# Optimization experiments

Measured on AMD Instinct MI355X. Metric: run time of the kernel, lower is better.

Reference implementation:

```python
import jax, jax.numpy as jnp
import numpy as np

N_NODES = 100000
N_EDGES = 1600000
NODE_DIM = 16
EDGE_DIM = 16
OUT_DIM = 16
H = 64  # edge/node/global hidden size
N_GRAPHS = 1


def _glorot(key, shape):
    fan_in, fan_out = shape[0], shape[1]
    lim = np.sqrt(6.0 / (fan_in + fan_out))
    return jax.random.uniform(key, shape, jnp.float32, -lim, lim)


def setup_inputs() -> dict:
    key = jax.random.key(0)
    ks = jax.random.split(key, 16)
    x = jax.random.normal(ks[0], (N_NODES, NODE_DIM), jnp.float32)
    edge_attr = jax.random.normal(ks[1], (N_EDGES, EDGE_DIM), jnp.float32)
    u = jax.random.normal(ks[2], (N_GRAPHS, H), jnp.float32)
    senders = jax.random.randint(ks[3], (N_EDGES,), 0, N_NODES, jnp.int32)
    receivers = jax.random.randint(ks[4], (N_EDGES,), 0, N_NODES, jnp.int32)
    node_gidx = jnp.zeros((N_NODES,), jnp.int32)
    edge_gidx = jnp.zeros((N_EDGES,), jnp.int32)
    # EdgeBlock MLP: in = edge + 2*node + global_h
    W_eb = _glorot(ks[5], (EDGE_DIM + 2 * NODE_DIM + H, H)); b_eb = jnp.zeros((H,), jnp.float32)
    # NodeBlock MLP: in = node + edge_h + global_h
    W_nb = _glorot(ks[6], (NODE_DIM + H + H, H)); b_nb = jnp.zeros((H,), jnp.float32)
    # GlobalBlock MLP: in = node_h + edge_h + global_h
    W_gb = _glorot(ks[7], (H + H + H, H)); b_gb = jnp.zeros((H,), jnp.float32)
    # node decoder: in = 2*edge_h + node_h + global_h -> H -> out
    W_d1 = _glorot(ks[8], (2 * H + H + H, H)); b_d1 = jnp.zeros((H,), jnp.float32)
    W_d2 = _glorot(ks[9], (H, OUT_DIM)); b_d2 = jnp.zeros((OUT_DIM,), jnp.float32)
    return dict(x=x, edge_attr=edge_attr, u=u, senders=senders, receivers=receivers,
                node_gidx=node_gidx, edge_gidx=edge_gidx,
                W_eb=W_eb, b_eb=b_eb, W_nb=W_nb, b_nb=b_nb, W_gb=W_gb, b_gb=b_gb,
                W_d1=W_d1, b_d1=b_d1, W_d2=W_d2, b_d2=b_d2)


def _segment_mean(data, ids, num_segments):
    s = jax.ops.segment_sum(data, ids, num_segments=num_segments)
    cnt = jax.ops.segment_sum(jnp.ones((data.shape[0], 1), data.dtype), ids, num_segments=num_segments)
    return s / jnp.maximum(cnt, 1.0)


def reference(x, edge_attr, u, senders, receivers, node_gidx, edge_gidx,
              W_eb, b_eb, W_nb, b_nb, W_gb, b_gb, W_d1, b_d1, W_d2, b_d2):
    # ---- GN1: EdgeBlock (gather -> concat -> linear+relu) ----
    e_in = jnp.concatenate([edge_attr, x[receivers], x[senders], u[edge_gidx]], axis=-1)  # [E, 112]
    e_h = jax.nn.relu(e_in @ W_eb + b_eb)  # [E, H]
    # ---- GN1: NodeBlock (scatter_add of received edges) ----
    agg_recv = jax.ops.segment_sum(e_h, receivers, num_segments=x.shape[0])  # [N, H]
    n_in = jnp.concatenate([agg_recv, x, u[node_gidx]], axis=-1)
    n_h = jax.nn.relu(n_in @ W_nb + b_nb)  # [N, H]
    # ---- GN1: GlobalBlock (scatter_mean reductions) ----
    e_mean = _segment_mean(e_h, edge_gidx, u.shape[0])  # [B, H]
    n_mean = _segment_mean(n_h, node_gidx, u.shape[0])  # [B, H]
    g_in = jnp.concatenate([e_mean, n_mean, u], axis=-1)
    u2 = jax.nn.relu(g_in @ W_gb + b_gb)  # [B, H]
    # ---- GN2: node decoder block (scatter_mean sent + received edges) ----
    agg_recv2 = _segment_mean(e_h, receivers, x.shape[0])
    agg_sent2 = _segment_mean(e_h, senders, x.shape[0])
    d_in = jnp.concatenate([agg_recv2, agg_sent2, n_h, u2[node_gidx]], axis=-1)  # [N, 256]
    out = jax.nn.relu(d_in @ W_d1 + b_d1) @ W_d2 + b_d2  # [N, out_dim]
    return out
```

## Files before the change

kernel.cpp:

```cpp
#include <hip/hip_runtime.h>


typedef unsigned int uint;
typedef unsigned short ushort;
typedef __attribute__((ext_vector_type(8))) short bf16x8;
typedef __attribute__((ext_vector_type(4))) float f32x4;

#define BW 128
#define BSHIFT 7
#define NBMAX 784
#define DC 8192
#define EMASK 0x1FFFFFu

#define LDF4(p) (*reinterpret_cast<const float4*>(p))

__device__ __forceinline__ ushort f2bf(float f) {
  uint u = __float_as_uint(f);
  u += 0x7FFFu + ((u >> 16) & 1u);
  return (ushort)(u >> 16);
}

__device__ __forceinline__ int aswz(int row, int kb) {
  return row * 64 + ((kb ^ (row & 7)) << 3);
}
__device__ __forceinline__ int nswz(int row, int kb) {
  return row * 128 + (((kb & 8) | ((kb ^ row) & 7)) << 3);
}
__device__ __forceinline__ int aswz192(int row, int kb) {
  return row * 192 + (((kb & 24) | ((kb ^ row) & 7)) << 3);
}

__global__ __launch_bounds__(256) void init_kernel(
    const float* __restrict__ x, ushort* __restrict__ xb, int n16,
    const float* __restrict__ u, const float* __restrict__ W_eb,
    const float* __restrict__ b_eb, const float* __restrict__ W_nb,
    const float* __restrict__ b_nb, const float* __restrict__ W_d1,
    const float* __restrict__ W_d2, float* __restrict__ eb_init,
    float* __restrict__ nb_init, ushort* __restrict__ wt_lin,
    ushort* __restrict__ wnb_img, ushort* __restrict__ wtd1_img,
    ushort* __restrict__ w2_img) {
  if (blockIdx.x == 0) {
    int j = threadIdx.x;
    if (j >= 64) return;
    float ae = b_eb[j], an = b_nb[j];
    for (int k = 0; k < 64; ++k) {
      float uk = u[k];
      ae = fmaf(uk, W_eb[(48 + k) * 64 + j], ae);
      an = fmaf(uk, W_nb[(80 + k) * 64 + j], an);
    }
    eb_init[j] = ae;
    nb_init[j] = an;
    for (int k = 0; k < 64; ++k)
      wt_lin[j * 64 + k] = (k < 48) ? f2bf(W_eb[k * 64 + j]) : (ushort)0;
    for (int k = 0; k < 128; ++k) {
      ushort v = (k < 80) ? f2bf(W_nb[k * 64 + j]) : (ushort)0;
      wnb_img[nswz(j, k >> 3) + (k & 7)] = v;
    }
    for (int k = 0; k < 192; ++k)
      wtd1_img[aswz192(j, k >> 3) + (k & 7)] = f2bf(W_d1[k * 64 + j]);
    if (j < 16)
      for (int k = 0; k < 64; ++k)
        w2_img[aswz(j, k >> 3) + (k & 7)] = f2bf(W_d2[k * 16 + j]);
    return;
  }
  int i = (blockIdx.x - 1) * 256 + threadIdx.x;
  if (i * 4 >= n16) return;
  float4 a = LDF4(x + i * 4);
  ushort4 o = {f2bf(a.x), f2bf(a.y), f2bf(a.z), f2bf(a.w)};
  *reinterpret_cast<ushort4*>(xb + i * 4) = o;
}

__global__ __launch_bounds__(256) void bcount_kernel(
    const int* __restrict__ receivers, const int* __restrict__ senders,
    uint* __restrict__ bcnt_r, uint* __restrict__ bcnt_s, int E, int NB) {
  __shared__ uint hr[NBMAX], hs[NBMAX];
  int t = threadIdx.x;
  for (int i = t; i < NB; i += 256) { hr[i] = 0; hs[i] = 0; }
  __syncthreads();
  int stride = gridDim.x * 256;
  for (int e = blockIdx.x * 256 + t; e < E; e += stride) {
    atomicAdd(&hr[receivers[e] >> BSHIFT], 1u);
    atomicAdd(&hs[senders[e] >> BSHIFT], 1u);
  }
  __syncthreads();
  for (int i = t; i < NB; i += 256) {
    if (hr[i]) atomicAdd(&bcnt_r[i], hr[i]);
    if (hs[i]) atomicAdd(&bcnt_s[i], hs[i]);
  }
}

__global__ __launch_bounds__(256) void bscan_kernel(
    const uint* __restrict__ bcnt_r, const uint* __restrict__ bcnt_s,
    uint* __restrict__ start_r, uint* __restrict__ start_s,
    uint* __restrict__ cur_r, uint* __restrict__ cur_s, int E, int NB) {
  __shared__ uint ts[256];
  int t = threadIdx.x;
  #pragma unroll
  for (int pass = 0; pass < 2; ++pass) {
    const uint* cnt = pass ? bcnt_s : bcnt_r;
    uint* start = pass ? start_s : start_r;
    uint* cur = pass ? cur_s : cur_r;
    uint loc[4]; uint tsum = 0;
    #pragma unroll
    for (int q = 0; q < 4; ++q) {
      int i = t * 4 + q;
      loc[q] = (i < NB) ? cnt[i] : 0;
      tsum += loc[q];
    }
    ts[t] = tsum;
    __syncthreads();
    for (int off = 1; off < 256; off <<= 1) {
      uint a = (t >= off) ? ts[t - off] : 0;
      __syncthreads();
      ts[t] += a;
      __syncthreads();
    }
    uint run = ts[t] - tsum;
    #pragma unroll
    for (int q = 0; q < 4; ++q) {
      int i = t * 4 + q;
      if (i < NB) { start[i] = run; cur[i] = run; run += loc[q]; }
    }
    if (t == 0) start[NB] = (uint)E;
    __syncthreads();
  }
}

__global__ __launch_bounds__(256) void distribute_kernel(
    const int* __restrict__ receivers, const int* __restrict__ senders,
    uint* __restrict__ gcur_r, uint* __restrict__ gcur_s,
    uint* __restrict__ tmp_r, uint* __restrict__ tmp_s, int E, int NB) {
  __shared__ uint hist[NBMAX], lstart[NBMAX], cur[NBMAX], gbase[NBMAX];
  __shared__ uint ids[DC];
  __shared__ ushort idsB[DC];
  __shared__ uint ts[256];
  int dir = blockIdx.x & 1;
  const int* key = dir ? senders : receivers;
  uint* g_cursor = dir ? gcur_s : gcur_r;
  uint* tmp = dir ? tmp_s : tmp_r;
  int t = threadIdx.x;
  int base = (blockIdx.x >> 1) * DC;
  int cact = min(DC, E - base);
  for (int i = t; i < NB; i += 256) hist[i] = 0;
  __syncthreads();
  for (int k = 0; k < DC / 256; ++k) {
    int j = k * 256 + t;
    if (j < cact) atomicAdd(&hist[key[base + j] >> BSHIFT], 1u);
  }
  __syncthreads();
  {
    uint loc[4]; uint tsum = 0;
    #pragma unroll
    for (int q = 0; q < 4; ++q) {
      int i = t * 4 + q;
      loc[q] = (i < NB) ? hist[i] : 0;
      tsum += loc[q];
    }
    ts[t] = tsum;
    __syncthreads();
    for (int off = 1; off < 256; off <<= 1) {
      uint a = (t >= off) ? ts[t - off] : 0;
      __syncthreads();
      ts[t] += a;
      __syncthreads();
    }
    uint run = ts[t] - tsum;
    #pragma unroll
    for (int q = 0; q < 4; ++q) {
      int i = t * 4 + q;
      if (i < NB) { lstart[i] = run; cur[i] = run; run += loc[q]; }
    }
  }
  __syncthreads();
  for (int i = t; i < NB; i += 256)
    if (hist[i]) gbase[i] = atomicAdd(&g_cursor[i], hist[i]);
  for (int k = 0; k < DC / 256; ++k) {
    int j = k * 256 + t;
    if (j < cact) {
      int e = base + j;
      int kk = key[e];
      uint b = (uint)(kk >> BSHIFT);
      uint slot = atomicAdd(&cur[b], 1u);
      ids[slot] = ((uint)(kk & (BW - 1)) << 21) | (uint)e;
      idsB[slot] = (ushort)b;
    }
  }
  __syncthreads();
  for (int j = t; j < cact; j += 256) {
    uint b2 = idsB[j];
    tmp[gbase[b2] + ((uint)j - lstart[b2])] = ids[j];
  }
}

__global__ __launch_bounds__(256) void bucketsort_kernel(
    const uint* __restrict__ tmp_r, const uint* __restrict__ tmp_s,
    const uint* __restrict__ start_r, const uint* __restrict__ start_s,
    uint* __restrict__ eidx_r, uint* __restrict__ eidx_s,
    uint* __restrict__ cnt_r, uint* __restrict__ cnt_s, int N) {
  __shared__ uint hist[BW], pfx[BW], cur[BW];
  int d = blockIdx.x & 1;
  int b = blockIdx.x >> 1;
  const uint* tmp = d ? tmp_s : tmp_r;
  const uint* start = d ? start_s : start_r;
  uint* eidx = d ? eidx_s : eidx_r;
  uint* cnt = d ? cnt_s : cnt_r;
  int t = threadIdx.x;
  if (t < BW) hist[t] = 0;
  __syncthreads();
  int beg = (int)start[b], end = (int)start[b + 1];
  for (int i = beg + t; i < end; i += 256) atomicAdd(&hist[tmp[i] >> 21], 1u);
  __syncthreads();
  if (t < BW) pfx[t] = hist[t];
  __syncthreads();
  for (int off = 1; off < BW; off <<= 1) {
    uint a = 0;
    if (t < BW && t >= off) a = pfx[t - off];
    __syncthreads();
    if (t < BW) pfx[t] += a;
    __syncthreads();
  }
  if (t < BW) cur[t] = pfx[t] - hist[t];
  __syncthreads();
  for (int i = beg + t; i < end; i += 256) {
    uint v = tmp[i];
    uint nl = v >> 21;
    uint p = atomicAdd(&cur[nl], 1u);
    eidx[beg + p] = v & EMASK;
  }
  int nbase = b * BW;
  if (t < BW && nbase + t < N) cnt[nbase + t] = hist[t];
}

__global__ __launch_bounds__(256, 4) void escatter_kernel(
    const float* __restrict__ edge_attr, const ushort* __restrict__ xb,
    const int* __restrict__ senders, const int* __restrict__ receivers,
    const uint* __restrict__ eidx_r, const uint* __restrict__ eidx_s,
    const ushort* __restrict__ wt_lin, const float* __restrict__ eb_init,
    float* __restrict__ sum_recv, float* __restrict__ sum_sent, int E,
    int ntiles) {
  __shared__ float Clds[4][16 * 72];
  __shared__ int nodeW[4][16];
  int t = threadIdx.x;
  int wid = t >> 6, l = t & 63;
  int lrow = l & 15, lk = l >> 4;
  bf16x8 b0[4], b1[4];
  float ebi[4];
  #pragma unroll
  for (int nt = 0; nt < 4; ++nt) {
    const ushort* wr = wt_lin + (nt * 16 + lrow) * 64;
    b0[nt] = *reinterpret_cast<const bf16x8*>(wr + lk * 8);
    b1[nt] = *reinterpret_cast<const bf16x8*>(wr + 32 + lk * 8);
    ebi[nt] = eb_init[nt * 16 + lrow];
  }
  const bf16x8 zero8 = {0, 0, 0, 0, 0, 0, 0, 0};
  int dir = blockIdx.x & 1;
  const uint* eidx = dir ? eidx_s : eidx_r;
  float* sum = dir ? sum_sent : sum_recv;
  int gw = (blockIdx.x >> 1) * 4 + wid;
  int nw = (gridDim.x >> 1) * 4;
  for (int tile = gw; tile < ntiles; tile += nw) {
    int m = tile * 16 + lrow;
    int mc = min(m, E - 1);
    int e = (int)eidx[mc];
    int r = receivers[e];
    int s = senders[e];
    if (lk == 0) nodeW[wid][lrow] = dir ? s : r;
    bf16x8 a0, a1;
    if (lk < 2) {
      const float* ap = edge_attr + (size_t)e * 16 + lk * 8;
      float4 f0 = LDF4(ap), f1 = LDF4(ap + 4);
      union { ushort h[8]; bf16x8 v; } pk;
      pk.h[0] = f2bf(f0.x); pk.h[1] = f2bf(f0.y);
      pk.h[2] = f2bf(f0.z); pk.h[3] = f2bf(f0.w);
      pk.h[4] = f2bf(f1.x); pk.h[5] = f2bf(f1.y);
      pk.h[6] = f2bf(f1.z); pk.h[7] = f2bf(f1.w);
      a0 = pk.v;
      a1 = *reinterpret_cast<const bf16x8*>(xb + (size_t)s * 16 + lk * 8);
    } else {
      a0 = *reinterpret_cast<const bf16x8*>(xb + (size_t)r * 16 +
                                            (lk - 2) * 8);
      a1 = zero8;
    }
    f32x4 acc[4];
    #pragma unroll
    for (int nt = 0; nt < 4; ++nt) {
      acc[nt] = f32x4{ebi[nt], ebi[nt], ebi[nt], ebi[nt]};
      acc[nt] =
          __builtin_amdgcn_mfma_f32_16x16x32_bf16(a0, b0[nt], acc[nt], 0, 0, 0);
      acc[nt] =
          __builtin_amdgcn_mfma_f32_16x16x32_bf16(a1, b1[nt], acc[nt], 0, 0, 0);
    }
    int m0 = (l >> 4) * 4;
    #pragma unroll
    for (int nt = 0; nt < 4; ++nt) {
      #pragma unroll
      for (int reg = 0; reg < 4; ++reg) {
        Clds[wid][(m0 + reg) * 72 + nt * 16 + lrow] =
            fmaxf(acc[nt][reg], 0.f);
      }
    }
    int vc = min(16, E - tile * 16);
    float accum = 0.f;
    int prev = nodeW[wid][0];
    for (int mm = 0; mm < vc; ++mm) {
      int nd = nodeW[wid][mm];
      float v = Clds[wid][mm * 72 + l];
      if (nd != prev) {
        atomicAdd(&sum[(size_t)prev * 64 + l], accum);
        accum = 0.f;
        prev = nd;
      }
      accum += v;
    }
    atomicAdd(&sum[(size_t)prev * 64 + l], accum);
  }
}

__global__ __launch_bounds__(256, 2) void node_mfma_kernel(
    const float* __restrict__ sum_recv, const ushort* __restrict__ xb,
    const ushort* __restrict__ wnb_img, const float* __restrict__ nb_init,
    ushort* __restrict__ n_h, int N) {
  __shared__ ushort Alds[64 * 128];
  __shared__ ushort Wlds[64 * 128];
  __shared__ ushort Clds[4][16 * 72];
  int t = threadIdx.x;
  int base = blockIdx.x * 64;
  {
    const uint4* src = reinterpret_cast<const uint4*>(wnb_img);
    uint4* dst = reinterpret_cast<uint4*>(Wlds);
    #pragma unroll
    for (int i = 0; i < 4; ++i) dst[t + 256 * i] = src[t + 256 * i];
  }
  {
    int m = t >> 2, part = t & 3;
    int n = base + m;
    bool val = n < N;
    if (part < 2) {
      #pragma unroll
      for (int q = 0; q < 4; ++q) {
        int c = part * 4 + q;
        union { ushort h[8]; uint4 qq; } pk;
        if (val) {
          const float* src = sum_recv + (size_t)n * 64 + c * 8;
          float4 f0 = LDF4(src), f1 = LDF4(src + 4);
          pk.h[0] = f2bf(f0.x); pk.h[1] = f2bf(f0.y);
          pk.h[2] = f2bf(f0.z); pk.h[3] = f2bf(f0.w);
          pk.h[4] = f2bf(f1.x); pk.h[5] = f2bf(f1.y);
          pk.h[6] = f2bf(f1.z); pk.h[7] = f2bf(f1.w);
        } else {
          pk.qq = uint4{0, 0, 0, 0};
        }
        *reinterpret_cast<uint4*>(&Alds[nswz(m, c)]) = pk.qq;
      }
    } else if (part == 2) {
      uint4 w0 = {0, 0, 0, 0}, w1 = {0, 0, 0, 0};
      if (val) {
        const uint4* xp = reinterpret_cast<const uint4*>(xb + (size_t)n * 16);
        w0 = xp[0]; w1 = xp[1];
      }
      *reinterpret_cast<uint4*>(&Alds[nswz(m, 8)]) = w0;
      *reinterpret_cast<uint4*>(&Alds[nswz(m, 9)]) = w1;
      *reinterpret_cast<uint4*>(&Alds[nswz(m, 10)]) = uint4{0, 0, 0, 0};
      *reinterpret_cast<uint4*>(&Alds[nswz(m, 11)]) = uint4{0, 0, 0, 0};
    } else {
      #pragma unroll
      for (int q = 0; q < 4; ++q)
        *reinterpret_cast<uint4*>(&Alds[nswz(m, 12 + q)]) = uint4{0, 0, 0, 0};
    }
  }
  __syncthreads();
  int wid = t >> 6, l = t & 63;
  int lrow = l & 15, lk = l >> 4;
  int arow = wid * 16 + lrow;
  bf16x8 afr[4];
  #pragma unroll
  for (int g = 0; g < 4; ++g)
    afr[g] = *reinterpret_cast<const bf16x8*>(&Alds[nswz(arow, g * 4 + lk)]);
  f32x4 acc[4];
  #pragma unroll
  for (int nt = 0; nt < 4; ++nt) {
    float nbi = nb_init[nt * 16 + lrow];
    acc[nt] = f32x4{nbi, nbi, nbi, nbi};
    #pragma unroll
    for (int g = 0; g < 4; ++g) {
      bf16x8 b = *reinterpret_cast<const bf16x8*>(
          &Wlds[nswz(nt * 16 + lrow, g * 4 + lk)]);
      acc[nt] =
          __builtin_amdgcn_mfma_f32_16x16x32_bf16(afr[g], b, acc[nt], 0, 0, 0);
    }
  }
  int m0 = (l >> 4) * 4;
  #pragma unroll
  for (int nt = 0; nt < 4; ++nt) {
    #pragma unroll
    for (int reg = 0; reg < 4; ++reg) {
      Clds[wid][(m0 + reg) * 72 + nt * 16 + lrow] =
          f2bf(fmaxf(acc[nt][reg], 0.f));
    }
  }
  __syncthreads();
  int sm = l >> 2, ch = l & 3;
  int gn = base + wid * 16 + sm;
  uint4 c0 = *reinterpret_cast<const uint4*>(&Clds[wid][sm * 72 + ch * 16]);
  uint4 c1 = *reinterpret_cast<const uint4*>(&Clds[wid][sm * 72 + ch * 16 + 8]);
  if (gn < N) {
    uint4* dst = reinterpret_cast<uint4*>(n_h + (size_t)gn * 64 + ch * 16);
    dst[0] = c0;
    dst[1] = c1;
  }
}

__global__ __launch_bounds__(256) void reduce_kernel(
    const float* __restrict__ sum_recv, const ushort* __restrict__ n_h,
    float* __restrict__ e_sum, float* __restrict__ n_sum, int N) {
  __shared__ float ls[128];
  if (threadIdx.x < 128) ls[threadIdx.x] = 0.f;
  __syncthreads();
  int g = threadIdx.x & 15;
  int tid = blockIdx.x * blockDim.x + threadIdx.x;
  int row0 = tid >> 4;
  int rstride = (gridDim.x * blockDim.x) >> 4;
  float pe[4] = {0, 0, 0, 0}, pn[4] = {0, 0, 0, 0};
  for (int r = row0; r < N; r += rstride) {
    float4 a = LDF4(sum_recv + (size_t)r * 64 + g * 4);
    uint2 b = *reinterpret_cast<const uint2*>(n_h + (size_t)r * 64 + g * 4);
    pe[0] += a.x; pe[1] += a.y; pe[2] += a.z; pe[3] += a.w;
    pn[0] += __uint_as_float(b.x << 16);
    pn[1] += __uint_as_float(b.x & 0xFFFF0000u);
    pn[2] += __uint_as_float(b.y << 16);
    pn[3] += __uint_as_float(b.y & 0xFFFF0000u);
  }
  #pragma unroll
  for (int i = 0; i < 4; ++i) {
    atomicAdd(&ls[g * 4 + i], pe[i]);
    atomicAdd(&ls[64 + g * 4 + i], pn[i]);
  }
  __syncthreads();
  if (threadIdx.x < 64) {
    atomicAdd(&e_sum[threadIdx.x], ls[threadIdx.x]);
    atomicAdd(&n_sum[threadIdx.x], ls[64 + threadIdx.x]);
  }
}

__global__ void global_kernel(const float* __restrict__ u,
                              const float* __restrict__ e_sum,
                              const float* __restrict__ n_sum,
                              const float* __restrict__ W_gb,
                              const float* __restrict__ b_gb,
                              const float* __restrict__ W_d1,
                              const float* __restrict__ b_d1,
                              float* __restrict__ d1_init, float Ef, float Nf) {
  __shared__ float gin[192];
  __shared__ float u2s[64];
  int j = threadIdx.x;
  gin[j] = e_sum[j] / Ef;
  gin[64 + j] = n_sum[j] / Nf;
  gin[128 + j] = u[j];
  __syncthreads();
  float a = b_gb[j];
  for (int k = 0; k < 192; ++k) a = fmaf(gin[k], W_gb[k * 64 + j], a);
  u2s[j] = fmaxf(a, 0.f);
  __syncthreads();
  float d = b_d1[j];
  for (int k = 0; k < 64; ++k) d = fmaf(u2s[k], W_d1[(192 + k) * 64 + j], d);
  d1_init[j] = d;
}

__global__ __launch_bounds__(256, 2) void decoder_mfma_kernel(
    const float* __restrict__ sum_recv, const float* __restrict__ sum_sent,
    const uint* __restrict__ cnt_r, const uint* __restrict__ cnt_s,
    const ushort* __restrict__ n_h, const ushort* __restrict__ wtd1_img,
    const float* __restrict__ d1_init, const ushort* __restrict__ w2_img,
    const float* __restrict__ b_d2, float* __restrict__ out, int N) {
  __shared__ ushort Alds[64 * 192];
  __shared__ ushort Wlds[64 * 192];
  __shared__ ushort Hlds[64 * 64];
  __shared__ ushort W2lds[16 * 64];
  int t = threadIdx.x;
  int base = blockIdx.x * 64;
  {
    const uint4* src = reinterpret_cast<const uint4*>(wtd1_img);
    uint4* dst = reinterpret_cast<uint4*>(Wlds);
    #pragma unroll
    for (int i = 0; i < 6; ++i) dst[t + 256 * i] = src[t + 256 * i];
    if (t < 128)
      reinterpret_cast<uint4*>(W2lds)[t] =
          reinterpret_cast<const uint4*>(w2_img)[t];
  }
  {
    int m = t >> 2;
    int n = base + m;
    bool val = n < N;
    float invr = 0.f, invs = 0.f;
    if (val) {
      invr = 1.f / fmaxf((float)cnt_r[n], 1.f);
      invs = 1.f / fmaxf((float)cnt_s[n], 1.f);
    }
    int c0 = (t & 3) * 6;
    for (int c = c0; c < c0 + 6; ++c) {
      union { ushort h[8]; uint4 q; } pk;
      if (val) {
        if (c >= 16) {
          pk.q = *reinterpret_cast<const uint4*>(n_h + (size_t)n * 64 +
                                                 (c - 16) * 8);
        } else {
          const float* src;
          float scl;
          if (c < 8) { src = sum_recv + (size_t)n * 64 + c * 8; scl = invr; }
          else       { src = sum_sent + (size_t)n * 64 + (c - 8) * 8; scl = invs; }
          float4 f0 = LDF4(src), f1 = LDF4(src + 4);
          pk.h[0] = f2bf(f0.x * scl); pk.h[1] = f2bf(f0.y * scl);
          pk.h[2] = f2bf(f0.z * scl); pk.h[3] = f2bf(f0.w * scl);
          pk.h[4] = f2bf(f1.x * scl); pk.h[5] = f2bf(f1.y * scl);
          pk.h[6] = f2bf(f1.z * scl); pk.h[7] = f2bf(f1.w * scl);
        }
      } else {
        pk.q = uint4{0, 0, 0, 0};
      }
      *reinterpret_cast<uint4*>(&Alds[aswz192(m, c)]) = pk.q;
    }
  }
  __syncthreads();
  int wid = t >> 6, l = t & 63;
  int lrow = l & 15, lk = l >> 4;
  int arow = wid * 16 + lrow;
  bf16x8 afr[6];
  #pragma unroll
  for (int g = 0; g < 6; ++g)
    afr[g] = *reinterpret_cast<const bf16x8*>(&Alds[aswz192(arow, g * 4 + lk)]);
  f32x4 acc[4];
  #pragma unroll
  for (int nt = 0; nt < 4; ++nt) {
    float di = d1_init[nt * 16 + lrow];
    acc[nt] = f32x4{di, di, di, di};
    #pragma unroll
    for (int g = 0; g < 6; ++g) {
      bf16x8 b = *reinterpret_cast<const bf16x8*>(
          &Wlds[aswz192(nt * 16 + lrow, g * 4 + lk)]);
      acc[nt] =
          __builtin_amdgcn_mfma_f32_16x16x32_bf16(afr[g], b, acc[nt], 0, 0, 0);
    }
  }
  int m0 = (l >> 4) * 4;
  #pragma unroll
  for (int nt = 0; nt < 4; ++nt) {
    #pragma unroll
    for (int reg = 0; reg < 4; ++reg) {
      int hm = wid * 16 + m0 + reg;
      int hn = nt * 16 + lrow;
      Hlds[hm * 64 + (((hn >> 3) ^ (hm & 7)) << 3) + (hn & 7)] =
          f2bf(fmaxf(acc[nt][reg], 0.f));
    }
  }
  __syncthreads();
  bf16x8 a20 = *reinterpret_cast<const bf16x8*>(&Hlds[aswz(arow, lk)]);
  bf16x8 a21 = *reinterpret_cast<const bf16x8*>(&Hlds[aswz(arow, 4 + lk)]);
  bf16x8 b20 = *reinterpret_cast<const bf16x8*>(&W2lds[aswz(lrow, lk)]);
  bf16x8 b21 = *reinterpret_cast<const bf16x8*>(&W2lds[aswz(lrow, 4 + lk)]);
  float bi = b_d2[lrow];
  f32x4 o = f32x4{bi, bi, bi, bi};
  o = __builtin_amdgcn_mfma_f32_16x16x32_bf16(a20, b20, o, 0, 0, 0);
  o = __builtin_amdgcn_mfma_f32_16x16x32_bf16(a21, b21, o, 0, 0, 0);
  #pragma unroll
  for (int reg = 0; reg < 4; ++reg) {
    int ge = base + wid * 16 + m0 + reg;
    if (ge < N) out[(size_t)ge * 16 + lrow] = o[reg];
  }
}

extern "C" void kernel_launch(void* const* d_in, const int* in_sizes, int n_in,
                              void* d_out, int out_size, void* d_ws,
                              size_t ws_size, hipStream_t stream) {
  const float* x         = (const float*)d_in[0];
  const float* edge_attr = (const float*)d_in[1];
  const float* u         = (const float*)d_in[2];
  const int*   senders   = (const int*)d_in[3];
  const int*   receivers = (const int*)d_in[4];
  const float* W_eb = (const float*)d_in[7];
  const float* b_eb = (const float*)d_in[8];
  const float* W_nb = (const float*)d_in[9];
  const float* b_nb = (const float*)d_in[10];
  const float* W_gb = (const float*)d_in[11];
  const float* b_gb = (const float*)d_in[12];
  const float* W_d1 = (const float*)d_in[13];
  const float* b_d1 = (const float*)d_in[14];
  const float* W_d2 = (const float*)d_in[15];
  const float* b_d2 = (const float*)d_in[16];

  int N = in_sizes[0] / 16;
  int E = in_sizes[1] / 16;
  int NB = (N + BW - 1) >> BSHIFT;
  int NDB = (E + DC - 1) / DC;
  int ntiles = (E + 15) / 16;

  char* w = (char*)d_ws;
  float* sum_recv = (float*)w;       w += (size_t)N * 64 * 4;
  float* sum_sent = (float*)w;       w += (size_t)N * 64 * 4;
  ushort* n_h = (ushort*)w;          w += (size_t)N * 64 * 2;
  uint* tmp_r = (uint*)w;            w += (size_t)E * 4;
  uint* tmp_s = (uint*)w;            w += (size_t)E * 4;
  uint* eidx_r = (uint*)w;           w += (size_t)E * 4;
  uint* eidx_s = (uint*)w;           w += (size_t)E * 4;
  uint* cnt_r = (uint*)w;            w += (size_t)N * 4;
  uint* cnt_s = (uint*)w;            w += (size_t)N * 4;
  ushort* xb = (ushort*)w;           w += (size_t)N * 16 * 2;
  ushort* wt_lin = (ushort*)w;       w += (size_t)64 * 64 * 2;
  ushort* wnb_img = (ushort*)w;      w += (size_t)64 * 128 * 2;
  ushort* wtd1_img = (ushort*)w;     w += (size_t)64 * 192 * 2;
  ushort* w2_img = (ushort*)w;       w += (size_t)16 * 64 * 2;
  uint* start_r = (uint*)w;          w += (size_t)(NB + 1) * 4;
  uint* start_s = (uint*)w;          w += (size_t)(NB + 1) * 4;
  uint* cur_r = (uint*)w;            w += (size_t)NB * 4;
  uint* cur_s = (uint*)w;            w += (size_t)NB * 4;
  uint* bcnt_r = (uint*)w;           w += (size_t)NBMAX * 4;
  uint* bcnt_s = (uint*)w;           w += (size_t)NBMAX * 4;
  float* e_sum = (float*)w;          w += 64 * 4;
  float* n_sum = (float*)w;          w += 64 * 4;
  float* eb_init = (float*)w;        w += 64 * 4;
  float* nb_init = (float*)w;        w += 64 * 4;
  float* d1_init = (float*)w;        w += 64 * 4;

  size_t zero_bytes = (size_t)(2 * NBMAX + 128) * 4;
  hipMemsetAsync(bcnt_r, 0, zero_bytes, stream);
  hipMemsetAsync(sum_recv, 0, (size_t)N * 128 * 4, stream);

  hipLaunchKernelGGL(init_kernel, dim3(1 + (N * 16 / 4 + 255) / 256), dim3(256),
                     0, stream, x, xb, N * 16, u, W_eb, b_eb, W_nb, b_nb, W_d1,
                     W_d2, eb_init, nb_init, wt_lin, wnb_img, wtd1_img, w2_img);
  hipLaunchKernelGGL(bcount_kernel, dim3(64), dim3(256), 0, stream, receivers,
                     senders, bcnt_r, bcnt_s, E, NB);
  hipLaunchKernelGGL(bscan_kernel, dim3(1), dim3(256), 0, stream, bcnt_r,
                     bcnt_s, start_r, start_s, cur_r, cur_s, E, NB);
  hipLaunchKernelGGL(distribute_kernel, dim3(2 * NDB), dim3(256), 0, stream,
                     receivers, senders, cur_r, cur_s, tmp_r, tmp_s, E, NB);
  hipLaunchKernelGGL(bucketsort_kernel, dim3(2 * NB), dim3(256), 0, stream,
                     tmp_r, tmp_s, start_r, start_s, eidx_r, eidx_s, cnt_r,
                     cnt_s, N);
  hipLaunchKernelGGL(escatter_kernel, dim3(2048), dim3(256), 0, stream,
                     edge_attr, xb, senders, receivers, eidx_r, eidx_s, wt_lin,
                     eb_init, sum_recv, sum_sent, E, ntiles);
  hipLaunchKernelGGL(node_mfma_kernel, dim3((N + 63) / 64), dim3(256), 0,
                     stream, sum_recv, xb, wnb_img, nb_init, n_h, N);
  hipLaunchKernelGGL(reduce_kernel, dim3(256), dim3(256), 0, stream, sum_recv,
                     n_h, e_sum, n_sum, N);
  hipLaunchKernelGGL(global_kernel, dim3(1), dim3(64), 0, stream, u, e_sum,
                     n_sum, W_gb, b_gb, W_d1, b_d1, d1_init, (float)E,
                     (float)N);
  hipLaunchKernelGGL(decoder_mfma_kernel, dim3((N + 63) / 64), dim3(256), 0,
                     stream, sum_recv, sum_sent, cnt_r, cnt_s, n_h, wtd1_img,
                     d1_init, w2_img, b_d2, (float*)d_out, N);
}
```

Measured before the change: 482.0 us.

## Carry sorted node ids through bucket sort to avoid random index gathers

The distribute and bucketsort kernels now carry the other endpoint node id next to each edge id. They write sorted key-node and other-node arrays, so the edge MLP scatter kernel reads both endpoints contiguously instead of doing dependent random gathers into receivers and senders. DC is halved to fit the larger uint2 shared buffer. This adds extra sequential writes and reads of the sort temporaries and doubles the distribute grid size.

```diff
diff --git a/kernel.cpp b/kernel.cpp
--- a/kernel.cpp
+++ b/kernel.cpp
@@ -9,7 +9,7 @@
 #define BW 128
 #define BSHIFT 7
 #define NBMAX 784
-#define DC 8192
+#define DC 4096
 #define EMASK 0x1FFFFFu
 
 #define LDF4(p) (*reinterpret_cast<const float4*>(p))
@@ -129,15 +129,16 @@
 __global__ __launch_bounds__(256) void distribute_kernel(
     const int* __restrict__ receivers, const int* __restrict__ senders,
     uint* __restrict__ gcur_r, uint* __restrict__ gcur_s,
-    uint* __restrict__ tmp_r, uint* __restrict__ tmp_s, int E, int NB) {
+    uint2* __restrict__ tmp_r, uint2* __restrict__ tmp_s, int E, int NB) {
   __shared__ uint hist[NBMAX], lstart[NBMAX], cur[NBMAX], gbase[NBMAX];
-  __shared__ uint ids[DC];
+  __shared__ uint2 ids[DC];
   __shared__ ushort idsB[DC];
   __shared__ uint ts[256];
   int dir = blockIdx.x & 1;
   const int* key = dir ? senders : receivers;
+  const int* oth = dir ? receivers : senders;
   uint* g_cursor = dir ? gcur_s : gcur_r;
-  uint* tmp = dir ? tmp_s : tmp_r;
+  uint2* tmp = dir ? tmp_s : tmp_r;
   int t = threadIdx.x;
   int base = (blockIdx.x >> 1) * DC;
   int cact = min(DC, E - base);
@@ -181,7 +182,8 @@
       int kk = key[e];
       uint b = (uint)(kk >> BSHIFT);
       uint slot = atomicAdd(&cur[b], 1u);
-      ids[slot] = ((uint)(kk & (BW - 1)) << 21) | (uint)e;
+      ids[slot] = uint2{((uint)(kk & (BW - 1)) << 21) | (uint)e,
+                        (uint)oth[e]};
       idsB[slot] = (ushort)b;
     }
   }
@@ -193,22 +195,27 @@
 }
 
 __global__ __launch_bounds__(256) void bucketsort_kernel(
-    const uint* __restrict__ tmp_r, const uint* __restrict__ tmp_s,
+    const uint2* __restrict__ tmp_r, const uint2* __restrict__ tmp_s,
     const uint* __restrict__ start_r, const uint* __restrict__ start_s,
     uint* __restrict__ eidx_r, uint* __restrict__ eidx_s,
+    uint* __restrict__ nkey_r, uint* __restrict__ nkey_s,
+    uint* __restrict__ noth_r, uint* __restrict__ noth_s,
     uint* __restrict__ cnt_r, uint* __restrict__ cnt_s, int N) {
   __shared__ uint hist[BW], pfx[BW], cur[BW];
   int d = blockIdx.x & 1;
   int b = blockIdx.x >> 1;
-  const uint* tmp = d ? tmp_s : tmp_r;
+  const uint2* tmp = d ? tmp_s : tmp_r;
   const uint* start = d ? start_s : start_r;
   uint* eidx = d ? eidx_s : eidx_r;
+  uint* nkey = d ? nkey_s : nkey_r;
+  uint* noth = d ? noth_s : noth_r;
   uint* cnt = d ? cnt_s : cnt_r;
   int t = threadIdx.x;
   if (t < BW) hist[t] = 0;
   __syncthreads();
   int beg = (int)start[b], end = (int)start[b + 1];
-  for (int i = beg + t; i < end; i += 256) atomicAdd(&hist[tmp[i] >> 21], 1u);
+  for (int i = beg + t; i < end; i += 256)
+    atomicAdd(&hist[tmp[i].x >> 21], 1u);
   __syncthreads();
   if (t < BW) pfx[t] = hist[t];
   __syncthreads();
@@ -221,20 +228,23 @@
   }
   if (t < BW) cur[t] = pfx[t] - hist[t];
   __syncthreads();
+  int nbase = b * BW;
   for (int i = beg + t; i < end; i += 256) {
-    uint v = tmp[i];
-    uint nl = v >> 21;
-    uint p = atomicAdd(&cur[nl], 1u);
-    eidx[beg + p] = v & EMASK;
-  }
-  int nbase = b * BW;
+    uint2 v = tmp[i];
+    uint nl = v.x >> 21;
+    uint p = beg + atomicAdd(&cur[nl], 1u);
+    eidx[p] = v.x & EMASK;
+    nkey[p] = (uint)nbase + nl;
+    noth[p] = v.y;
+  }
   if (t < BW && nbase + t < N) cnt[nbase + t] = hist[t];
 }
 
 __global__ __launch_bounds__(256, 4) void escatter_kernel(
     const float* __restrict__ edge_attr, const ushort* __restrict__ xb,
-    const int* __restrict__ senders, const int* __restrict__ receivers,
-    const uint* __restrict__ eidx_r, const uint* __restrict__ eidx_s,
+    const uint* __restrict__ eidx_r, const uint* __restrict__ nkey_r,
+    const uint* __restrict__ noth_r, const uint* __restrict__ eidx_s,
+    const uint* __restrict__ nkey_s, const uint* __restrict__ noth_s,
     const ushort* __restrict__ wt_lin, const float* __restrict__ eb_init,
     float* __restrict__ sum_recv, float* __restrict__ sum_sent, int E,
     int ntiles) {
@@ -255,6 +265,8 @@
   const bf16x8 zero8 = {0, 0, 0, 0, 0, 0, 0, 0};
   int dir = blockIdx.x & 1;
   const uint* eidx = dir ? eidx_s : eidx_r;
+  const uint* nkey = dir ? nkey_s : nkey_r;
+  const uint* noth = dir ? noth_s : noth_r;
   float* sum = dir ? sum_sent : sum_recv;
   int gw = (blockIdx.x >> 1) * 4 + wid;
   int nw = (gridDim.x >> 1) * 4;
@@ -262,9 +274,11 @@
     int m = tile * 16 + lrow;
     int mc = min(m, E - 1);
     int e = (int)eidx[mc];
-    int r = receivers[e];
-    int s = senders[e];
-    if (lk == 0) nodeW[wid][lrow] = dir ? s : r;
+    int kn = (int)nkey[mc];
+    int on = (int)noth[mc];
+    int s = dir ? kn : on;
+    int r = dir ? on : kn;
+    if (lk == 0) nodeW[wid][lrow] = kn;
     bf16x8 a0, a1;
     if (lk < 2) {
       const float* ap = edge_attr + (size_t)e * 16 + lk * 8;
@@ -597,10 +611,14 @@
   float* sum_recv = (float*)w;       w += (size_t)N * 64 * 4;
   float* sum_sent = (float*)w;       w += (size_t)N * 64 * 4;
   ushort* n_h = (ushort*)w;          w += (size_t)N * 64 * 2;
-  uint* tmp_r = (uint*)w;            w += (size_t)E * 4;
-  uint* tmp_s = (uint*)w;            w += (size_t)E * 4;
+  uint2* tmp_r = (uint2*)w;          w += (size_t)E * 8;
+  uint2* tmp_s = (uint2*)w;          w += (size_t)E * 8;
   uint* eidx_r = (uint*)w;           w += (size_t)E * 4;
   uint* eidx_s = (uint*)w;           w += (size_t)E * 4;
+  uint* nkey_r = (uint*)w;           w += (size_t)E * 4;
+  uint* nkey_s = (uint*)w;           w += (size_t)E * 4;
+  uint* noth_r = (uint*)w;           w += (size_t)E * 4;
+  uint* noth_s = (uint*)w;           w += (size_t)E * 4;
   uint* cnt_r = (uint*)w;            w += (size_t)N * 4;
   uint* cnt_s = (uint*)w;            w += (size_t)N * 4;
   ushort* xb = (ushort*)w;           w += (size_t)N * 16 * 2;
@@ -634,11 +652,11 @@
   hipLaunchKernelGGL(distribute_kernel, dim3(2 * NDB), dim3(256), 0, stream,
                      receivers, senders, cur_r, cur_s, tmp_r, tmp_s, E, NB);
   hipLaunchKernelGGL(bucketsort_kernel, dim3(2 * NB), dim3(256), 0, stream,
-                     tmp_r, tmp_s, start_r, start_s, eidx_r, eidx_s, cnt_r,
-                     cnt_s, N);
+                     tmp_r, tmp_s, start_r, start_s, eidx_r, eidx_s, nkey_r,
+                     nkey_s, noth_r, noth_s, cnt_r, cnt_s, N);
   hipLaunchKernelGGL(escatter_kernel, dim3(2048), dim3(256), 0, stream,
-                     edge_attr, xb, senders, receivers, eidx_r, eidx_s, wt_lin,
-                     eb_init, sum_recv, sum_sent, E, ntiles);
+                     edge_attr, xb, eidx_r, nkey_r, noth_r, eidx_s, nkey_s,
+                     noth_s, wt_lin, eb_init, sum_recv, sum_sent, E, ntiles);
   hipLaunchKernelGGL(node_mfma_kernel, dim3((N + 63) / 64), dim3(256), 0,
                      stream, sum_recv, xb, wnb_img, nb_init, n_h, N);
   hipLaunchKernelGGL(reduce_kernel, dim3(256), dim3(256), 0, stream, sum_recv,
```

Result: no change. 486.3 us (+0.9%).
